# Kernel optimization log

Measured on AMD Instinct MI355X. Metric: run time of the kernel, lower is better.

Reference implementation:

```python
import jax, jax.numpy as jnp
import numpy as np

B, T, N, F = 16, 12, 1000, 64
K_CHEB, OUT = 3, 64


def setup_inputs() -> dict:
    key = jax.random.key(0)
    k1, k2, k3, k4 = jax.random.split(key, 4)
    x = jax.random.normal(k1, (B, T, N, F), dtype=jnp.float32)
    SAtt = jax.random.uniform(k2, (B, N, N), dtype=jnp.float32)
    cheb = jax.random.normal(k3, (K_CHEB, N, N), dtype=jnp.float32) * 0.05
    Theta = jax.random.normal(k4, (K_CHEB, F, OUT), dtype=jnp.float32) * 0.05
    return {"x": x, "SAtt": SAtt, "cheb": cheb, "Theta": Theta}


def reference(x, SAtt, cheb, Theta):
    # Attention-masked Chebyshev polynomials: A[b,k,i,j] = cheb[k,i,j] * SAtt[b,i,j]
    A = cheb[None, :, :, :] * SAtt[:, None, :, :]          # (B,K,N,N)
    # rhs[b,t,k,i,f] = sum_j A[b,k,j,i] * x[b,t,j,f]  (transpose of A in original code)
    rhs = jnp.einsum('bkji,btjf->btkif', A, x)             # (B,T,K,N,F)
    # accumulate over k with per-k feature transform Theta[k]
    out = jnp.einsum('btkif,kfo->btio', rhs, Theta)        # (B,T,N,OUT)
    return jax.nn.relu(out)
```

## Files before the change

kernel.cpp:

```cpp
#include <hip/hip_runtime.h>

#define B_  16
#define T_  12
#define N_  1000
#define F_  64
#define KC  3
#define O_  64
#define NP  1024
#define KP  (KC * NP)
#define CC  (T_ * O_)

typedef __bf16 bf16x8 __attribute__((ext_vector_type(8)));
typedef float  f32x4  __attribute__((ext_vector_type(4)));

__device__ __forceinline__ unsigned short f2bf(float f) {
  __bf16 h = (__bf16)f;
  return __builtin_bit_cast(unsigned short, h);
}

__device__ __forceinline__ void gl_lds16(const void* g, void* l) {
  __builtin_amdgcn_global_load_lds(
      (const __attribute__((address_space(1))) unsigned int*)g,
      (__attribute__((address_space(3))) unsigned int*)l,
      16, 0, 0);
}

__global__ __launch_bounds__(256) void k_prep(
    const float* __restrict__ x, const float* __restrict__ SAtt,
    const float* __restrict__ cheb, const float* __restrict__ Theta,
    unsigned short* __restrict__ ASt, unsigned short* __restrict__ Yt) {
  __shared__ union {
    struct { unsigned short prod[KC][64][66]; } s1;
    struct {
      unsigned short thl[KC][64][72];
      unsigned short xl[64][72];
      unsigned short ot[64][72];
    } s2;
  } sm;
  const int tid = threadIdx.x;
  const int bid = blockIdx.x;

  if (bid < 4096) {
    const int ib = (bid & 15) * 64, jb = ((bid >> 4) & 15) * 64, b = bid >> 8;
    const int ii4 = (tid & 15) * 4, jr = tid >> 4;
#pragma unroll
    for (int p = 0; p < 4; ++p) {
      const int jj = p * 16 + jr;
      const int gj = jb + jj;
      const int gjc = gj < N_ ? gj : N_ - 1;
      const int gi = ib + ii4;
      const bool iok = gi < N_;
      const bool ok = iok && (gj < N_);
      float4 s4 = make_float4(0.f, 0.f, 0.f, 0.f);
      if (iok) s4 = *(const float4*)&SAtt[((size_t)b * N_ + gjc) * N_ + gi];
#pragma unroll
      for (int k = 0; k < KC; ++k) {
        float4 c4 = make_float4(0.f, 0.f, 0.f, 0.f);
        if (iok) c4 = *(const float4*)&cheb[((size_t)k * N_ + gjc) * N_ + gi];
        ushort2 lo, hi;
        lo.x = ok ? f2bf(c4.x * s4.x) : (unsigned short)0;
        lo.y = ok ? f2bf(c4.y * s4.y) : (unsigned short)0;
        hi.x = ok ? f2bf(c4.z * s4.z) : (unsigned short)0;
        hi.y = ok ? f2bf(c4.w * s4.w) : (unsigned short)0;
        *(ushort2*)&sm.s1.prod[k][jj][ii4]     = lo;
        *(ushort2*)&sm.s1.prod[k][jj][ii4 + 2] = hi;
      }
    }
    __syncthreads();
    const int j8 = (tid & 7) * 8, i0 = tid >> 3;
#pragma unroll
    for (int p = 0; p < 2; ++p) {
      const int iw = p * 32 + i0;
#pragma unroll
      for (int k = 0; k < KC; ++k) {
        unsigned short v[8];
#pragma unroll
        for (int m = 0; m < 8; ++m) v[m] = sm.s1.prod[k][j8 + m][iw];
        *(uint4*)&ASt[((size_t)(b * NP + ib + iw) * KC + k) * NP + jb + j8] =
            *(uint4*)v;
      }
    }
  } else {
    const int b2 = bid - 4096;
    const int jb = (b2 & 15) * 64, bt = b2 >> 4;
#pragma unroll
    for (int it = 0; it < 12; ++it) {
      const int e = (tid + it * 256) * 4;
      const int k = e >> 12, f = (e >> 6) & 63, o0 = e & 63;
      const float4 v = *(const float4*)&Theta[e];
      sm.s2.thl[k][o0 + 0][f] = f2bf(v.x);
      sm.s2.thl[k][o0 + 1][f] = f2bf(v.y);
      sm.s2.thl[k][o0 + 2][f] = f2bf(v.z);
      sm.s2.thl[k][o0 + 3][f] = f2bf(v.w);
    }
    const float* xrow = x + ((size_t)bt * N_ + jb) * F_;
#pragma unroll
    for (int p = 0; p < 4; ++p) {
      const int i4 = tid + p * 256;
      const int fl = i4 * 4, j = fl >> 6, f = fl & 63;
      float4 v;
      if (jb + j < N_) v = ((const float4*)xrow)[i4];
      else             v = make_float4(0.f, 0.f, 0.f, 0.f);
      ushort4 u;
      u.x = f2bf(v.x); u.y = f2bf(v.y); u.z = f2bf(v.z); u.w = f2bf(v.w);
      *(ushort4*)&sm.s2.xl[j][f] = u;
    }
    __syncthreads();

    const int w = tid >> 6, l = tid & 63, quad = l >> 4, lr = l & 15;
    const int os = tid >> 2, q = tid & 3;
#pragma unroll
    for (int k = 0; k < KC; ++k) {
      f32x4 acc[4];
#pragma unroll
      for (int mi = 0; mi < 4; ++mi) acc[mi] = (f32x4){0.f, 0.f, 0.f, 0.f};
#pragma unroll
      for (int ks = 0; ks < 2; ++ks) {
        const int fo = ks * 32 + quad * 8;
        const bf16x8 bb = *(const bf16x8*)&sm.s2.xl[w * 16 + lr][fo];
#pragma unroll
        for (int mi = 0; mi < 4; ++mi) {
          const bf16x8 a = *(const bf16x8*)&sm.s2.thl[k][mi * 16 + lr][fo];
          acc[mi] =
              __builtin_amdgcn_mfma_f32_16x16x32_bf16(a, bb, acc[mi], 0, 0, 0);
        }
      }
      __syncthreads();
#pragma unroll
      for (int mi = 0; mi < 4; ++mi)
#pragma unroll
        for (int r = 0; r < 4; ++r)
          sm.s2.ot[mi * 16 + quad * 4 + r][w * 16 + lr] = f2bf(acc[mi][r]);
      __syncthreads();
      unsigned short* yrow = &Yt[((size_t)(bt * O_ + os) * KC + k) * NP + jb];
      *(uint4*)&yrow[q * 8]      = *(const uint4*)&sm.s2.ot[os][q * 8];
      *(uint4*)&yrow[32 + q * 8] = *(const uint4*)&sm.s2.ot[os][32 + q * 8];
    }
  }
}

__global__ __launch_bounds__(256, 4) void k_gemm(
    const unsigned short* __restrict__ ASt, const unsigned short* __restrict__ Yt,
    float* __restrict__ out) {
  __shared__ unsigned short Al[128 * 64];
  __shared__ unsigned short Bl[96 * 64];
  const int tid = threadIdx.x;
  const int bid = blockIdx.x;
  const int xcd = bid & 7, s = bid >> 3;
  const int b = xcd * 2 + (s >> 6);
  const int r = s & 63;
  const int ib = (r >> 3) * 128, cb = (r & 7) * 96;

  const unsigned short* Abase = ASt + ((size_t)b * NP + ib) * KP;
  const unsigned short* Bbase = Yt + ((size_t)b * CC + cb) * KP;
  const int w = tid >> 6, l = tid & 63, quad = l >> 4, lr = l & 15;
  const int wr = w & 1, wc = w >> 1;
  const int lrow = l >> 3, lchunk = l & 7;
  const int src_chunk = lchunk ^ lrow;
  const int p0 = quad ^ (lr & 7);

  f32x4 acc[4][3];
#pragma unroll
  for (int mi = 0; mi < 4; ++mi)
#pragma unroll
    for (int ci = 0; ci < 3; ++ci)
      acc[mi][ci] = (f32x4){0.f, 0.f, 0.f, 0.f};

  for (int kt = 0; kt < KP / 64; ++kt) {
    __syncthreads();
    const int k0 = kt * 64;
#pragma unroll
    for (int s4 = 0; s4 < 4; ++s4) {
      const int row = w * 32 + s4 * 8;
      gl_lds16(Abase + (size_t)(row + lrow) * KP + k0 + src_chunk * 8,
               &Al[row * 64]);
    }
#pragma unroll
    for (int s4 = 0; s4 < 3; ++s4) {
      const int row = w * 24 + s4 * 8;
      gl_lds16(Bbase + (size_t)(row + lrow) * KP + k0 + src_chunk * 8,
               &Bl[row * 64]);
    }
    __syncthreads();
#pragma unroll
    for (int ks = 0; ks < 2; ++ks) {
      const int pc = (p0 ^ (ks * 4)) * 8;
      bf16x8 a[4], bb[3];
#pragma unroll
      for (int mi = 0; mi < 4; ++mi)
        a[mi] = *(const bf16x8*)&Al[(wr * 64 + mi * 16 + lr) * 64 + pc];
#pragma unroll
      for (int ci = 0; ci < 3; ++ci)
        bb[ci] = *(const bf16x8*)&Bl[(wc * 48 + ci * 16 + lr) * 64 + pc];
#pragma unroll
      for (int mi = 0; mi < 4; ++mi)
#pragma unroll
        for (int ci = 0; ci < 3; ++ci)
          acc[mi][ci] = __builtin_amdgcn_mfma_f32_16x16x32_bf16(
              a[mi], bb[ci], acc[mi][ci], 0, 0, 0);
    }
  }

#pragma unroll
  for (int mi = 0; mi < 4; ++mi) {
    const int i = ib + wr * 64 + mi * 16 + quad * 4;
#pragma unroll
    for (int ci = 0; ci < 3; ++ci) {
      const int c = cb + wc * 48 + ci * 16 + lr;
      const int t = c >> 6, o = c & 63;
#pragma unroll
      for (int r2 = 0; r2 < 4; ++r2) {
        if (i + r2 < N_) {
          const float v = acc[mi][ci][r2];
          out[((size_t)(b * T_ + t) * N_ + (i + r2)) * O_ + o] = v > 0.f ? v : 0.f;
        }
      }
    }
  }
}

extern "C" void kernel_launch(void* const* d_in, const int* in_sizes, int n_in,
                              void* d_out, int out_size, void* d_ws, size_t ws_size,
                              hipStream_t stream) {
  const float* x     = (const float*)d_in[0];
  const float* SAtt  = (const float*)d_in[1];
  const float* cheb  = (const float*)d_in[2];
  const float* Theta = (const float*)d_in[3];
  float* out = (float*)d_out;

  unsigned short* ASt = (unsigned short*)d_ws;
  unsigned short* Yt  = ASt + (size_t)B_ * NP * KC * NP;

  k_prep<<<4096 + 3072, 256, 0, stream>>>(x, SAtt, cheb, Theta, ASt, Yt);
  k_gemm<<<1024, 256, 0, stream>>>(ASt, Yt, out);
}
```

Baseline: 342.6 us.

## Switch GEMM to 32x32x16 MFMA with 128x128 block tiles

Replaces the 16x16x32 MFMA tiling with 32x32x16 bf16 MFMA, and grows the per-block tile from 128x96 to 128x128. This cuts the grid from 1024 to 768 blocks and lowers the occupancy hint from 4 to 2. The aim is more arithmetic per LDS read and fewer instructions per MAC. The cost is more accumulator registers per wave and fewer resident waves, which can hide memory latency less well. The output store mapping and LDS swizzle are rewritten to match the 32x32 accumulator layout.

```diff
diff --git a/kernel.cpp b/kernel.cpp
--- a/kernel.cpp
+++ b/kernel.cpp
@@ -12,6 +12,7 @@
 
 typedef __bf16 bf16x8 __attribute__((ext_vector_type(8)));
 typedef float  f32x4  __attribute__((ext_vector_type(4)));
+typedef float  f32x16 __attribute__((ext_vector_type(16)));
 
 __device__ __forceinline__ unsigned short f2bf(float f) {
   __bf16 h = (__bf16)f;
@@ -139,32 +140,34 @@
   }
 }
 
-__global__ __launch_bounds__(256, 4) void k_gemm(
+__global__ __launch_bounds__(256, 2) void k_gemm(
     const unsigned short* __restrict__ ASt, const unsigned short* __restrict__ Yt,
     float* __restrict__ out) {
   __shared__ unsigned short Al[128 * 64];
-  __shared__ unsigned short Bl[96 * 64];
+  __shared__ unsigned short Bl[128 * 64];
   const int tid = threadIdx.x;
   const int bid = blockIdx.x;
   const int xcd = bid & 7, s = bid >> 3;
-  const int b = xcd * 2 + (s >> 6);
-  const int r = s & 63;
-  const int ib = (r >> 3) * 128, cb = (r & 7) * 96;
+  const int b = xcd * 2 + (s / 48);
+  const int r48 = s % 48;
+  const int ib = (r48 / 6) * 128, cb = (r48 % 6) * 128;
 
   const unsigned short* Abase = ASt + ((size_t)b * NP + ib) * KP;
   const unsigned short* Bbase = Yt + ((size_t)b * CC + cb) * KP;
-  const int w = tid >> 6, l = tid & 63, quad = l >> 4, lr = l & 15;
+  const int w = tid >> 6, l = tid & 63;
+  const int l32 = l & 31, lh = l >> 5;
   const int wr = w & 1, wc = w >> 1;
   const int lrow = l >> 3, lchunk = l & 7;
   const int src_chunk = lchunk ^ lrow;
-  const int p0 = quad ^ (lr & 7);
-
-  f32x4 acc[4][3];
-#pragma unroll
-  for (int mi = 0; mi < 4; ++mi)
-#pragma unroll
-    for (int ci = 0; ci < 3; ++ci)
-      acc[mi][ci] = (f32x4){0.f, 0.f, 0.f, 0.f};
+
+  f32x16 acc[2][2];
+#pragma unroll
+  for (int mi = 0; mi < 2; ++mi)
+#pragma unroll
+    for (int ci = 0; ci < 2; ++ci)
+      acc[mi][ci] = (f32x16){0.f};
+
+  const int swz = l32 & 7;
 
   for (int kt = 0; kt < KP / 64; ++kt) {
     __syncthreads();
@@ -176,43 +179,45 @@
                &Al[row * 64]);
     }
 #pragma unroll
-    for (int s4 = 0; s4 < 3; ++s4) {
-      const int row = w * 24 + s4 * 8;
+    for (int s4 = 0; s4 < 4; ++s4) {
+      const int row = w * 32 + s4 * 8;
       gl_lds16(Bbase + (size_t)(row + lrow) * KP + k0 + src_chunk * 8,
                &Bl[row * 64]);
     }
     __syncthreads();
 #pragma unroll
-    for (int ks = 0; ks < 2; ++ks) {
-      const int pc = (p0 ^ (ks * 4)) * 8;
-      bf16x8 a[4], bb[3];
-#pragma unroll
-      for (int mi = 0; mi < 4; ++mi)
-        a[mi] = *(const bf16x8*)&Al[(wr * 64 + mi * 16 + lr) * 64 + pc];
-#pragma unroll
-      for (int ci = 0; ci < 3; ++ci)
-        bb[ci] = *(const bf16x8*)&Bl[(wc * 48 + ci * 16 + lr) * 64 + pc];
-#pragma unroll
-      for (int mi = 0; mi < 4; ++mi)
-#pragma unroll
-        for (int ci = 0; ci < 3; ++ci)
-          acc[mi][ci] = __builtin_amdgcn_mfma_f32_16x16x32_bf16(
+    for (int ks = 0; ks < 4; ++ks) {
+      const int chunk = ks * 2 + lh;
+      const int pc = (chunk ^ swz) * 8;
+      bf16x8 a[2], bb[2];
+#pragma unroll
+      for (int mi = 0; mi < 2; ++mi)
+        a[mi] = *(const bf16x8*)&Al[(wr * 64 + mi * 32 + l32) * 64 + pc];
+#pragma unroll
+      for (int ci = 0; ci < 2; ++ci)
+        bb[ci] = *(const bf16x8*)&Bl[(wc * 64 + ci * 32 + l32) * 64 + pc];
+#pragma unroll
+      for (int mi = 0; mi < 2; ++mi)
+#pragma unroll
+        for (int ci = 0; ci < 2; ++ci)
+          acc[mi][ci] = __builtin_amdgcn_mfma_f32_32x32x16_bf16(
               a[mi], bb[ci], acc[mi][ci], 0, 0, 0);
     }
   }
 
 #pragma unroll
-  for (int mi = 0; mi < 4; ++mi) {
-    const int i = ib + wr * 64 + mi * 16 + quad * 4;
-#pragma unroll
-    for (int ci = 0; ci < 3; ++ci) {
-      const int c = cb + wc * 48 + ci * 16 + lr;
+  for (int mi = 0; mi < 2; ++mi) {
+#pragma unroll
+    for (int ci = 0; ci < 2; ++ci) {
+      const int c = cb + wc * 64 + ci * 32 + l32;
       const int t = c >> 6, o = c & 63;
-#pragma unroll
-      for (int r2 = 0; r2 < 4; ++r2) {
-        if (i + r2 < N_) {
-          const float v = acc[mi][ci][r2];
-          out[((size_t)(b * T_ + t) * N_ + (i + r2)) * O_ + o] = v > 0.f ? v : 0.f;
+      float* orow = out + ((size_t)(b * T_ + t) * N_) * O_ + o;
+#pragma unroll
+      for (int r = 0; r < 16; ++r) {
+        const int i = ib + wr * 64 + mi * 32 + (r & 3) + 8 * (r >> 2) + 4 * lh;
+        if (i < N_) {
+          const float v = acc[mi][ci][r];
+          orow[(size_t)i * O_] = v > 0.f ? v : 0.f;
         }
       }
     }
@@ -232,5 +237,5 @@
   unsigned short* Yt  = ASt + (size_t)B_ * NP * KC * NP;
 
   k_prep<<<4096 + 3072, 256, 0, stream>>>(x, SAtt, cheb, Theta, ASt, Yt);
-  k_gemm<<<1024, 256, 0, stream>>>(ASt, Yt, out);
-}
+  k_gemm<<<768, 256, 0, stream>>>(ASt, Yt, out);
+}
```

Measured after the change: 326.6 us. 4.6% less time.
